# Kernel optimization log

Hardware: AMD Instinct MI355X
Metric: run time of the kernel (lower is better)

The kernel has to match this reference:

```python
import jax, jax.numpy as jnp
import numpy as np

N_NODES = 50000
N_EDGES = 800000
D = 128
E_DIM = 32
N_LAYERS = 4
BN_EPS = 1e-5


def setup_inputs() -> dict:
    key = jax.random.key(0)
    ks = jax.random.split(key, 9)
    return {
        "x": jax.random.normal(ks[0], (N_NODES, D), dtype=jnp.float32),
        "edge_attr": jax.random.normal(ks[1], (N_EDGES, E_DIM), dtype=jnp.float32),
        "edge_index": jax.random.randint(ks[2], (2, N_EDGES), 0, N_NODES, dtype=jnp.int64),
        "W_edge": jax.random.normal(ks[3], (N_LAYERS, E_DIM, D), dtype=jnp.float32) * 0.1,
        "b_edge": jnp.zeros((N_LAYERS, D), dtype=jnp.float32),
        "W1": jax.random.normal(ks[4], (N_LAYERS, D, D), dtype=jnp.float32) * 0.1,
        "b1": jnp.zeros((N_LAYERS, D), dtype=jnp.float32),
        "W2": jax.random.normal(ks[5], (N_LAYERS, D, D), dtype=jnp.float32) * 0.1,
        "b2": jnp.zeros((N_LAYERS, D), dtype=jnp.float32),
        "gamma": jnp.ones((N_LAYERS, D), dtype=jnp.float32),
        "beta": jnp.zeros((N_LAYERS, D), dtype=jnp.float32),
    }


def reference(x, edge_attr, edge_index, W_edge, b_edge, W1, b1, W2, b2, gamma, beta):
    src, dst = edge_index[0], edge_index[1]
    n = x.shape[0]
    for i in range(N_LAYERS):
        # GINEConv: message = ReLU(x_src + Lin(edge_attr)); scatter-add to dst
        e = edge_attr @ W_edge[i] + b_edge[i]            # [E, D]
        m = jax.nn.relu(x[src] + e)                      # [E, D]
        agg = jax.ops.segment_sum(m, dst, num_segments=n)  # [N, D]
        h = x + agg                                      # (1+eps)*x, eps=0
        # 2-layer MLP
        h = jax.nn.relu(h @ W1[i] + b1[i]) @ W2[i] + b2[i]
        # BatchNorm (training-mode batch stats, biased var) + ReLU; dropout off
        mean = h.mean(axis=0)
        var = h.var(axis=0)
        h = (h - mean) * jax.lax.rsqrt(var + BN_EPS) * gamma[i] + beta[i]
        x = jax.nn.relu(h)
    return x
```

## Files before the change

### kernel.cpp

```cpp
#include <hip/hip_runtime.h>

#define NN 50000
#define NE 800000
#define DD 128
#define ED 32
#define NL 4
#define BN_EPS 1e-5f
#define SCAN_B 1024
#define NB ((NN + SCAN_B - 1) / SCAN_B)
#define EB 128
#define MR 32

typedef __attribute__((ext_vector_type(8))) short bf16x8;
typedef __attribute__((ext_vector_type(4))) float f32x4;

__device__ __forceinline__ unsigned short f2bf(float f) {
    unsigned u = __float_as_uint(f);
    u += 0x7fffu + ((u >> 16) & 1u);
    return (unsigned short)(u >> 16);
}
__device__ __forceinline__ float bf2f(unsigned short h) {
    return __uint_as_float((unsigned)h << 16);
}

__global__ __launch_bounds__(256) void hist_kernel(
    const int* __restrict__ edst, int* __restrict__ deg)
{
    const int e = blockIdx.x * 256 + threadIdx.x;
    if (e < NE) atomicAdd(&deg[edst[e]], 1);
}

__global__ __launch_bounds__(256) void scan1_kernel(
    const int* __restrict__ deg, int* __restrict__ rowptr, int* __restrict__ bsum)
{
    __shared__ int sh[256];
    const int t = threadIdx.x, b = blockIdx.x;
    const int base = b * SCAN_B + t * 4;
    int v[4];
#pragma unroll
    for (int j = 0; j < 4; ++j) {
        const int idx = base + j;
        v[j] = (idx < NN) ? deg[idx] : 0;
    }
    sh[t] = v[0] + v[1] + v[2] + v[3];
    __syncthreads();
    for (int off = 1; off < 256; off <<= 1) {
        const int val = (t >= off) ? sh[t - off] : 0;
        __syncthreads();
        sh[t] += val;
        __syncthreads();
    }
    int p = (t == 0) ? 0 : sh[t - 1];
#pragma unroll
    for (int j = 0; j < 4; ++j) {
        const int idx = base + j;
        if (idx < NN) rowptr[idx] = p;
        p += v[j];
    }
    if (t == 255) bsum[b] = sh[255];
}

__global__ void scan2_kernel(int* __restrict__ bsum)
{
    if (threadIdx.x == 0) {
        int acc = 0;
        for (int i = 0; i < NB; ++i) { const int v = bsum[i]; bsum[i] = acc; acc += v; }
    }
}

__global__ __launch_bounds__(256) void scan3_kernel(
    int* __restrict__ rowptr, int* __restrict__ cursor, const int* __restrict__ bsum)
{
    const int idx = blockIdx.x * 256 + threadIdx.x;
    if (idx < NN) {
        const int v = rowptr[idx] + bsum[idx / SCAN_B];
        rowptr[idx] = v;
        cursor[idx] = v;
    }
    if (idx == 0) rowptr[NN] = NE;
}

__global__ __launch_bounds__(256) void scatter_kernel(
    const int* __restrict__ esrc, const int* __restrict__ edst,
    const float* __restrict__ ea, int* __restrict__ cursor,
    int2* __restrict__ sd_perm, unsigned short* __restrict__ ea_bf)
{
    const int e = blockIdx.x * 256 + threadIdx.x;
    if (e < NE) {
        const int d = edst[e];
        const int pos = atomicAdd(&cursor[d], 1);
        sd_perm[pos] = make_int2(esrc[e], d);
        const float* er = &ea[(size_t)e * ED];
        unsigned short* ob = &ea_bf[(size_t)pos * ED];
#pragma unroll
        for (int g = 0; g < 8; ++g) {
            const float4 v = *(const float4*)&er[g * 4];
            uint2 p;
            p.x = (unsigned)f2bf(v.x) | ((unsigned)f2bf(v.y) << 16);
            p.y = (unsigned)f2bf(v.z) | ((unsigned)f2bf(v.w) << 16);
            *(uint2*)&ob[g * 4] = p;
        }
    }
}

__global__ __launch_bounds__(256) void wconv_kernel(
    const float* __restrict__ We, unsigned short* __restrict__ wtb)
{
    const int tid = blockIdx.x * 256 + threadIdx.x;
    if (tid < NL * DD * ED) {
        const int l = tid / (DD * ED);
        const int r = tid % (DD * ED);
        const int c = r / ED, k = r % ED;
        wtb[tid] = f2bf(We[(size_t)l * ED * DD + k * DD + c]);
    }
}

__global__ __launch_bounds__(256) void w12conv_kernel(
    const float* __restrict__ W1, const float* __restrict__ W2,
    unsigned short* __restrict__ w1t, unsigned short* __restrict__ w2t)
{
    const int tid = blockIdx.x * 256 + threadIdx.x;
    if (tid < NL * DD * DD) {
        const int l = tid / (DD * DD);
        const int r = tid % (DD * DD);
        const int n = r / DD, k = r % DD;
        const size_t s = (size_t)l * DD * DD + k * DD + n;
        w1t[tid] = f2bf(W1[s]);
        w2t[tid] = f2bf(W2[s]);
    }
}

__global__ __launch_bounds__(256, 5) void edge_mfma_kernel(
    const float* __restrict__ x,
    const unsigned short* __restrict__ eab,
    const int2* __restrict__ sd_perm,
    const unsigned short* __restrict__ wtb,
    const float* __restrict__ be,
    float* __restrict__ agg)
{
    __shared__ unsigned short msgl[EB * 128];
    const int t = threadIdx.x;
    const int wv = t >> 6, ln = t & 63;
    const int l15 = ln & 15, kb = ln >> 4;
    const int e0 = blockIdx.x * EB;

    const int c0 = (2 * wv + 0) * 16 + l15;
    const int c1 = (2 * wv + 1) * 16 + l15;
    const bf16x8 bfr0 = *(const bf16x8*)&wtb[c0 * ED + kb * 8];
    const bf16x8 bfr1 = *(const bf16x8*)&wtb[c1 * ED + kb * 8];

#pragma unroll
    for (int eg = 0; eg < EB / 16; ++eg) {
        const int edge = eg * 16 + l15;
        const bf16x8 afr = *(const bf16x8*)&eab[(size_t)(e0 + edge) * ED + kb * 8];
        f32x4 z = {0.f, 0.f, 0.f, 0.f};
        const f32x4 d0 = __builtin_amdgcn_mfma_f32_16x16x32_bf16(afr, bfr0, z, 0, 0, 0);
        const f32x4 d1 = __builtin_amdgcn_mfma_f32_16x16x32_bf16(afr, bfr1, z, 0, 0, 0);
#pragma unroll
        for (int j = 0; j < 4; ++j) {
            const int mrow = eg * 16 + kb * 4 + j;
            const int sw = ((mrow >> 2) & 3) << 3;
            const int i0 = (((c0 >> 1) ^ sw) << 1) | (c0 & 1);
            const int i1 = (((c1 >> 1) ^ sw) << 1) | (c1 & 1);
            msgl[mrow * 128 + i0] = f2bf(d0[j]);
            msgl[mrow * 128 + i1] = f2bf(d1[j]);
        }
    }
    __syncthreads();

    const int lbase = wv * 32;
    const int2* sdp = &sd_perm[e0 + lbase];
    const int c2 = ln * 2;
    const float2 bv = *(const float2*)&be[c2];
    float2 acc = {0.f, 0.f};
    int seg_start = 0;
#pragma unroll 1
    for (int g = 0; g < 4; ++g) {
        const int gb = g * 8;
        int4 pr[4];
#pragma unroll
        for (int q = 0; q < 4; ++q)
            pr[q] = *(const int4*)&sdp[gb + 2 * q];
        const int srcs[8] = {pr[0].x, pr[0].z, pr[1].x, pr[1].z,
                             pr[2].x, pr[2].z, pr[3].x, pr[3].z};
        int dsts[9];
        dsts[0] = pr[0].y; dsts[1] = pr[0].w; dsts[2] = pr[1].y; dsts[3] = pr[1].w;
        dsts[4] = pr[2].y; dsts[5] = pr[2].w; dsts[6] = pr[3].y; dsts[7] = pr[3].w;
        dsts[8] = (gb + 8 < 32) ? sdp[gb + 8].y : -1;
        float2 xv[8];
#pragma unroll
        for (int q = 0; q < 8; ++q)
            xv[q] = *(const float2*)&x[(size_t)srcs[q] * DD + c2];
#pragma unroll
        for (int q = 0; q < 8; ++q) {
            const int i = gb + q;
            const int dw = ln ^ (((i >> 2) & 3) << 3);
            const unsigned mm = *(const unsigned*)&msgl[(lbase + i) * 128 + dw * 2];
            const float mlo = __uint_as_float(mm << 16);
            const float mhi = __uint_as_float(mm & 0xffff0000u);
            acc.x += fmaxf(xv[q].x + mlo + bv.x, 0.f);
            acc.y += fmaxf(xv[q].y + mhi + bv.y, 0.f);
            if (i == 31 || dsts[q + 1] != dsts[q]) {
                float* ap = &agg[(size_t)dsts[q] * DD + c2];
                if (seg_start > 0 && i < 31) {
                    *(float2*)ap = acc;
                } else {
                    unsafeAtomicAdd(ap + 0, acc.x);
                    unsafeAtomicAdd(ap + 1, acc.y);
                }
                acc.x = 0.f; acc.y = 0.f;
                seg_start = i + 1;
            }
        }
    }
}

__global__ __launch_bounds__(256, 5) void mlp_mfma_kernel(
    const float* __restrict__ x, const float* __restrict__ agg,
    float* __restrict__ h2out,
    const unsigned short* __restrict__ w1t,
    const unsigned short* __restrict__ w2t,
    const float* __restrict__ b1, const float* __restrict__ b2,
    float* __restrict__ bns)
{
    __shared__ unsigned short ah[MR * 128];
    __shared__ unsigned short al[MR * 128];
    __shared__ unsigned short bh[MR * 128];
    __shared__ unsigned short bl[MR * 128];
    const int t = threadIdx.x;
    const int wv = t >> 6, ln = t & 63, l15 = ln & 15, kb = ln >> 4;
    const int r0 = blockIdx.x * MR;

#pragma unroll
    for (int p = 0; p < 2; ++p) {
        const int row = p * 16 + (t >> 4);
        const int gc = t & 15;
        const int grow = r0 + row;
        float v[8] = {0.f, 0.f, 0.f, 0.f, 0.f, 0.f, 0.f, 0.f};
        if (grow < NN) {
            const size_t g = (size_t)grow * DD + gc * 8;
            const float4 xa = *(const float4*)&x[g];
            const float4 xc = *(const float4*)&x[g + 4];
            const float4 ga = *(const float4*)&agg[g];
            const float4 gc4 = *(const float4*)&agg[g + 4];
            v[0] = xa.x + ga.x; v[1] = xa.y + ga.y; v[2] = xa.z + ga.z; v[3] = xa.w + ga.w;
            v[4] = xc.x + gc4.x; v[5] = xc.y + gc4.y; v[6] = xc.z + gc4.z; v[7] = xc.w + gc4.w;
        }
        unsigned hiw[4], low[4];
#pragma unroll
        for (int j = 0; j < 4; ++j) {
            const unsigned short h0 = f2bf(v[2 * j]);
            const unsigned short h1 = f2bf(v[2 * j + 1]);
            const unsigned short q0 = f2bf(v[2 * j] - bf2f(h0));
            const unsigned short q1 = f2bf(v[2 * j + 1] - bf2f(h1));
            hiw[j] = (unsigned)h0 | ((unsigned)h1 << 16);
            low[j] = (unsigned)q0 | ((unsigned)q1 << 16);
        }
        const int off = row * 128 + (gc ^ (row & 7)) * 8;
        *(uint4*)&ah[off] = *(uint4*)hiw;
        *(uint4*)&al[off] = *(uint4*)low;
    }

    bf16x8 w1f[2][4];
#pragma unroll
    for (int nt = 0; nt < 2; ++nt) {
        const int n = wv * 32 + nt * 16 + l15;
#pragma unroll
        for (int ks = 0; ks < 4; ++ks)
            w1f[nt][ks] = *(const bf16x8*)&w1t[n * DD + ks * 32 + kb * 8];
    }
    const int cA = wv * 32 + l15, cB = wv * 32 + 16 + l15;
    const float b1v[2] = {b1[cA], b1[cB]};
    const float b2v[2] = {b2[cA], b2[cB]};
    __syncthreads();

    f32x4 acc[2][2];
#pragma unroll
    for (int mt = 0; mt < 2; ++mt)
#pragma unroll
        for (int nt = 0; nt < 2; ++nt)
            acc[mt][nt] = (f32x4){0.f, 0.f, 0.f, 0.f};
#pragma unroll
    for (int ks = 0; ks < 4; ++ks) {
#pragma unroll
        for (int mt = 0; mt < 2; ++mt) {
            const int row = mt * 16 + l15;
            const int off = row * 128 + ((ks * 4 + kb) ^ (row & 7)) * 8;
            const bf16x8 afh = *(const bf16x8*)&ah[off];
            const bf16x8 afl = *(const bf16x8*)&al[off];
#pragma unroll
            for (int nt = 0; nt < 2; ++nt) {
                acc[mt][nt] = __builtin_amdgcn_mfma_f32_16x16x32_bf16(afh, w1f[nt][ks], acc[mt][nt], 0, 0, 0);
                acc[mt][nt] = __builtin_amdgcn_mfma_f32_16x16x32_bf16(afl, w1f[nt][ks], acc[mt][nt], 0, 0, 0);
            }
        }
    }

#pragma unroll
    for (int mt = 0; mt < 2; ++mt) {
#pragma unroll
        for (int nt = 0; nt < 2; ++nt) {
            const int col = wv * 32 + nt * 16 + l15;
#pragma unroll
            for (int j = 0; j < 4; ++j) {
                const int row = mt * 16 + kb * 4 + j;
                const float v = fmaxf(acc[mt][nt][j] + b1v[nt], 0.f);
                const unsigned short hi = f2bf(v);
                const int off = row * 128 + ((col >> 3) ^ (row & 7)) * 8 + (col & 7);
                bh[off] = hi;
                bl[off] = f2bf(v - bf2f(hi));
            }
        }
    }

    bf16x8 w2f[2][4];
#pragma unroll
    for (int nt = 0; nt < 2; ++nt) {
        const int n = wv * 32 + nt * 16 + l15;
#pragma unroll
        for (int ks = 0; ks < 4; ++ks)
            w2f[nt][ks] = *(const bf16x8*)&w2t[n * DD + ks * 32 + kb * 8];
    }
    __syncthreads();

#pragma unroll
    for (int mt = 0; mt < 2; ++mt)
#pragma unroll
        for (int nt = 0; nt < 2; ++nt)
            acc[mt][nt] = (f32x4){0.f, 0.f, 0.f, 0.f};
#pragma unroll
    for (int ks = 0; ks < 4; ++ks) {
#pragma unroll
        for (int mt = 0; mt < 2; ++mt) {
            const int row = mt * 16 + l15;
            const int off = row * 128 + ((ks * 4 + kb) ^ (row & 7)) * 8;
            const bf16x8 afh = *(const bf16x8*)&bh[off];
            const bf16x8 afl = *(const bf16x8*)&bl[off];
#pragma unroll
            for (int nt = 0; nt < 2; ++nt) {
                acc[mt][nt] = __builtin_amdgcn_mfma_f32_16x16x32_bf16(afh, w2f[nt][ks], acc[mt][nt], 0, 0, 0);
                acc[mt][nt] = __builtin_amdgcn_mfma_f32_16x16x32_bf16(afl, w2f[nt][ks], acc[mt][nt], 0, 0, 0);
            }
        }
    }

    float ps[2] = {0.f, 0.f}, pq[2] = {0.f, 0.f};
#pragma unroll
    for (int mt = 0; mt < 2; ++mt) {
#pragma unroll
        for (int nt = 0; nt < 2; ++nt) {
            const int col = wv * 32 + nt * 16 + l15;
#pragma unroll
            for (int j = 0; j < 4; ++j) {
                const int row = r0 + mt * 16 + kb * 4 + j;
                const float v = acc[mt][nt][j] + b2v[nt];
                if (row < NN) {
                    h2out[(size_t)row * DD + col] = v;
                    ps[nt] += v;
                    pq[nt] += v * v;
                }
            }
        }
    }
#pragma unroll
    for (int nt = 0; nt < 2; ++nt) {
        ps[nt] += __shfl_xor(ps[nt], 16);
        ps[nt] += __shfl_xor(ps[nt], 32);
        pq[nt] += __shfl_xor(pq[nt], 16);
        pq[nt] += __shfl_xor(pq[nt], 32);
    }
    if (kb == 0) {
#pragma unroll
        for (int nt = 0; nt < 2; ++nt) {
            const int col = wv * 32 + nt * 16 + l15;
            unsafeAtomicAdd(&bns[col], ps[nt]);
            unsafeAtomicAdd(&bns[DD + col], pq[nt]);
        }
    }
}

__global__ __launch_bounds__(256) void bn_apply(
    const float* __restrict__ h2, const float* __restrict__ bns,
    const float* __restrict__ gamma, const float* __restrict__ beta,
    float* __restrict__ xout)
{
    const size_t i = ((size_t)blockIdx.x * 256 + threadIdx.x) * 4;
    if (i >= (size_t)NN * DD) return;
    const int c4 = (int)(i & 127);
    const float4 hv = *(const float4*)&h2[i];
    const float4 sv = *(const float4*)&bns[c4];
    const float4 qv = *(const float4*)&bns[DD + c4];
    const float4 gv = *(const float4*)&gamma[c4];
    const float4 bv = *(const float4*)&beta[c4];
    const float inv_n = 1.f / (float)NN;
    float4 ov;
    {
        const float m = sv.x * inv_n;
        const float var = qv.x * inv_n - m * m;
        ov.x = fmaxf((hv.x - m) * __frsqrt_rn(var + BN_EPS) * gv.x + bv.x, 0.f);
    }
    {
        const float m = sv.y * inv_n;
        const float var = qv.y * inv_n - m * m;
        ov.y = fmaxf((hv.y - m) * __frsqrt_rn(var + BN_EPS) * gv.y + bv.y, 0.f);
    }
    {
        const float m = sv.z * inv_n;
        const float var = qv.z * inv_n - m * m;
        ov.z = fmaxf((hv.z - m) * __frsqrt_rn(var + BN_EPS) * gv.z + bv.z, 0.f);
    }
    {
        const float m = sv.w * inv_n;
        const float var = qv.w * inv_n - m * m;
        ov.w = fmaxf((hv.w - m) * __frsqrt_rn(var + BN_EPS) * gv.w + bv.w, 0.f);
    }
    *(float4*)&xout[i] = ov;
}

extern "C" void kernel_launch(void* const* d_in, const int* in_sizes, int n_in,
                              void* d_out, int out_size, void* d_ws, size_t ws_size,
                              hipStream_t stream) {
    const float* x0    = (const float*)d_in[0];
    const float* ea    = (const float*)d_in[1];
    const int*   eidx  = (const int*)d_in[2];
    const float* We    = (const float*)d_in[3];
    const float* be    = (const float*)d_in[4];
    const float* W1    = (const float*)d_in[5];
    const float* b1    = (const float*)d_in[6];
    const float* W2    = (const float*)d_in[7];
    const float* b2    = (const float*)d_in[8];
    const float* gamma = (const float*)d_in[9];
    const float* beta  = (const float*)d_in[10];
    float* out = (float*)d_out;
    float* ws  = (float*)d_ws;

    float* agg = ws;
    float* xb  = agg + (size_t)NN * DD;
    float* bns = xb + (size_t)NN * DD;
    int* deg      = (int*)(bns + 256);
    int* rowptr   = deg + 50000;
    int* cursor   = rowptr + 50004;
    int* bsum     = cursor + 50000;
    int2* sd_perm = (int2*)(bsum + 64);
    unsigned short* ea_bf = (unsigned short*)(sd_perm + NE);
    unsigned short* wt_bf = ea_bf + (size_t)NE * ED;
    unsigned short* w1t   = wt_bf + (size_t)NL * DD * ED;
    unsigned short* w2t   = w1t + (size_t)NL * DD * DD;

    const int* esrc = eidx;
    const int* edst = eidx + NE;

    hipMemsetAsync(deg, 0, NN * sizeof(int), stream);
    hist_kernel<<<(NE + 255) / 256, 256, 0, stream>>>(edst, deg);
    scan1_kernel<<<NB, 256, 0, stream>>>(deg, rowptr, bsum);
    scan2_kernel<<<1, 64, 0, stream>>>(bsum);
    scan3_kernel<<<(NN + 255) / 256, 256, 0, stream>>>(rowptr, cursor, bsum);
    scatter_kernel<<<(NE + 255) / 256, 256, 0, stream>>>(
        esrc, edst, ea, cursor, sd_perm, ea_bf);
    wconv_kernel<<<(NL * DD * ED + 255) / 256, 256, 0, stream>>>(We, wt_bf);
    w12conv_kernel<<<(NL * DD * DD + 255) / 256, 256, 0, stream>>>(W1, W2, w1t, w2t);

    const float* xcur = x0;
    for (int l = 0; l < NL; ++l) {
        hipMemsetAsync(agg, 0, (size_t)NN * DD * sizeof(float), stream);
        hipMemsetAsync(bns, 0, 2 * DD * sizeof(float), stream);
        edge_mfma_kernel<<<NE / EB, 256, 0, stream>>>(
            xcur, ea_bf, sd_perm,
            wt_bf + (size_t)l * DD * ED, be + (size_t)l * DD, agg);
        mlp_mfma_kernel<<<(NN + MR - 1) / MR, 256, 0, stream>>>(
            xcur, agg, agg,
            w1t + (size_t)l * DD * DD, w2t + (size_t)l * DD * DD,
            b1 + (size_t)l * DD, b2 + (size_t)l * DD, bns);
        float* xn = (l == NL - 1) ? out : xb;
        bn_apply<<<(NN * DD / 4 + 255) / 256, 256, 0, stream>>>(
            agg, bns, gamma + (size_t)l * DD, beta + (size_t)l * DD, xn);
        xcur = xn;
    }
}
```

Baseline: 714.3 us.

## Store node features in bf16 and split edge-attr permutation into gather pass

Node features between layers are now stored as bf16, so the random per-edge source gathers in the edge kernel and the row reads in the MLP kernel move half the bytes. The final layer still writes fp32 output. The edge-attribute permutation is split into an index scatter plus a separate coalesced gather kernel that uses eight threads per edge. This adds two extra kernels and lowers the precision of inputs to each layer, which risks accuracy drift across four layers.

```diff
diff --git a/kernel.cpp b/kernel.cpp
--- a/kernel.cpp
+++ b/kernel.cpp
@@ -80,27 +80,48 @@
     if (idx == 0) rowptr[NN] = NE;
 }
 
-__global__ __launch_bounds__(256) void scatter_kernel(
+__global__ __launch_bounds__(256) void scatter_idx_kernel(
     const int* __restrict__ esrc, const int* __restrict__ edst,
-    const float* __restrict__ ea, int* __restrict__ cursor,
-    int2* __restrict__ sd_perm, unsigned short* __restrict__ ea_bf)
+    int* __restrict__ cursor, int2* __restrict__ sd_perm, int* __restrict__ eid_perm)
 {
     const int e = blockIdx.x * 256 + threadIdx.x;
     if (e < NE) {
         const int d = edst[e];
         const int pos = atomicAdd(&cursor[d], 1);
         sd_perm[pos] = make_int2(esrc[e], d);
-        const float* er = &ea[(size_t)e * ED];
-        unsigned short* ob = &ea_bf[(size_t)pos * ED];
-#pragma unroll
-        for (int g = 0; g < 8; ++g) {
-            const float4 v = *(const float4*)&er[g * 4];
-            uint2 p;
-            p.x = (unsigned)f2bf(v.x) | ((unsigned)f2bf(v.y) << 16);
-            p.y = (unsigned)f2bf(v.z) | ((unsigned)f2bf(v.w) << 16);
-            *(uint2*)&ob[g * 4] = p;
-        }
-    }
+        eid_perm[pos] = e;
+    }
+}
+
+__global__ __launch_bounds__(256) void ea_gather_kernel(
+    const float* __restrict__ ea, const int* __restrict__ eid_perm,
+    unsigned short* __restrict__ ea_bf)
+{
+    const int tid = blockIdx.x * 256 + threadIdx.x;
+    const int pos = tid >> 3, j = tid & 7;
+    if (pos < NE) {
+        const int e = eid_perm[pos];
+        const float4 v = *(const float4*)&ea[(size_t)e * ED + j * 4];
+        uint2 p;
+        p.x = (unsigned)f2bf(v.x) | ((unsigned)f2bf(v.y) << 16);
+        p.y = (unsigned)f2bf(v.z) | ((unsigned)f2bf(v.w) << 16);
+        *(uint2*)&ea_bf[(size_t)pos * ED + j * 4] = p;
+    }
+}
+
+__global__ __launch_bounds__(256) void x0conv_kernel(
+    const float* __restrict__ x0, unsigned short* __restrict__ xbf)
+{
+    const size_t i = ((size_t)blockIdx.x * 256 + threadIdx.x) * 8;
+    if (i >= (size_t)NN * DD) return;
+    const float4 a = *(const float4*)&x0[i];
+    const float4 b = *(const float4*)&x0[i + 4];
+    uint4 o;
+    o.x = (unsigned)f2bf(a.x) | ((unsigned)f2bf(a.y) << 16);
+    o.y = (unsigned)f2bf(a.z) | ((unsigned)f2bf(a.w) << 16);
+    o.z = (unsigned)f2bf(b.x) | ((unsigned)f2bf(b.y) << 16);
+    o.w = (unsigned)f2bf(b.z) | ((unsigned)f2bf(b.w) << 16);
+    *(uint4*)&xbf[i] = o;
 }
 
 __global__ __launch_bounds__(256) void wconv_kernel(
@@ -131,7 +152,7 @@
 }
 
 __global__ __launch_bounds__(256, 5) void edge_mfma_kernel(
-    const float* __restrict__ x,
+    const unsigned short* __restrict__ xbf,
     const unsigned short* __restrict__ eab,
     const int2* __restrict__ sd_perm,
     const unsigned short* __restrict__ wtb,
@@ -189,8 +210,11 @@
         dsts[8] = (gb + 8 < 32) ? sdp[gb + 8].y : -1;
         float2 xv[8];
 #pragma unroll
-        for (int q = 0; q < 8; ++q)
-            xv[q] = *(const float2*)&x[(size_t)srcs[q] * DD + c2];
+        for (int q = 0; q < 8; ++q) {
+            const unsigned xu = *(const unsigned*)&xbf[(size_t)srcs[q] * DD + c2];
+            xv[q].x = __uint_as_float(xu << 16);
+            xv[q].y = __uint_as_float(xu & 0xffff0000u);
+        }
 #pragma unroll
         for (int q = 0; q < 8; ++q) {
             const int i = gb + q;
@@ -216,7 +240,7 @@
 }
 
 __global__ __launch_bounds__(256, 5) void mlp_mfma_kernel(
-    const float* __restrict__ x, const float* __restrict__ agg,
+    const unsigned short* __restrict__ xbf, const float* __restrict__ agg,
     float* __restrict__ h2out,
     const unsigned short* __restrict__ w1t,
     const unsigned short* __restrict__ w2t,
@@ -239,12 +263,17 @@
         float v[8] = {0.f, 0.f, 0.f, 0.f, 0.f, 0.f, 0.f, 0.f};
         if (grow < NN) {
             const size_t g = (size_t)grow * DD + gc * 8;
-            const float4 xa = *(const float4*)&x[g];
-            const float4 xc = *(const float4*)&x[g + 4];
+            const uint4 xu = *(const uint4*)&xbf[g];
             const float4 ga = *(const float4*)&agg[g];
-            const float4 gc4 = *(const float4*)&agg[g + 4];
-            v[0] = xa.x + ga.x; v[1] = xa.y + ga.y; v[2] = xa.z + ga.z; v[3] = xa.w + ga.w;
-            v[4] = xc.x + gc4.x; v[5] = xc.y + gc4.y; v[6] = xc.z + gc4.z; v[7] = xc.w + gc4.w;
+            const float4 gb4 = *(const float4*)&agg[g + 4];
+            v[0] = __uint_as_float(xu.x << 16)          + ga.x;
+            v[1] = __uint_as_float(xu.x & 0xffff0000u)  + ga.y;
+            v[2] = __uint_as_float(xu.y << 16)          + ga.z;
+            v[3] = __uint_as_float(xu.y & 0xffff0000u)  + ga.w;
+            v[4] = __uint_as_float(xu.z << 16)          + gb4.x;
+            v[5] = __uint_as_float(xu.z & 0xffff0000u)  + gb4.y;
+            v[6] = __uint_as_float(xu.w << 16)          + gb4.z;
+            v[7] = __uint_as_float(xu.w & 0xffff0000u)  + gb4.w;
         }
         unsigned hiw[4], low[4];
 #pragma unroll
@@ -379,7 +408,36 @@
     }
 }
 
-__global__ __launch_bounds__(256) void bn_apply(
+__global__ __launch_bounds__(256) void bn_apply_bf16(
+    const float* __restrict__ h2, const float* __restrict__ bns,
+    const float* __restrict__ gamma, const float* __restrict__ beta,
+    unsigned short* __restrict__ xout)
+{
+    const size_t i = ((size_t)blockIdx.x * 256 + threadIdx.x) * 4;
+    if (i >= (size_t)NN * DD) return;
+    const int c4 = (int)(i & 127);
+    const float4 hv = *(const float4*)&h2[i];
+    const float4 sv = *(const float4*)&bns[c4];
+    const float4 qv = *(const float4*)&bns[DD + c4];
+    const float4 gv = *(const float4*)&gamma[c4];
+    const float4 bv = *(const float4*)&beta[c4];
+    const float inv_n = 1.f / (float)NN;
+    float o0, o1, o2, o3;
+    { const float m = sv.x * inv_n; const float var = qv.x * inv_n - m * m;
+      o0 = fmaxf((hv.x - m) * __frsqrt_rn(var + BN_EPS) * gv.x + bv.x, 0.f); }
+    { const float m = sv.y * inv_n; const float var = qv.y * inv_n - m * m;
+      o1 = fmaxf((hv.y - m) * __frsqrt_rn(var + BN_EPS) * gv.y + bv.y, 0.f); }
+    { const float m = sv.z * inv_n; const float var = qv.z * inv_n - m * m;
+      o2 = fmaxf((hv.z - m) * __frsqrt_rn(var + BN_EPS) * gv.z + bv.z, 0.f); }
+    { const float m = sv.w * inv_n; const float var = qv.w * inv_n - m * m;
+      o3 = fmaxf((hv.w - m) * __frsqrt_rn(var + BN_EPS) * gv.w + bv.w, 0.f); }
+    uint2 o;
+    o.x = (unsigned)f2bf(o0) | ((unsigned)f2bf(o1) << 16);
+    o.y = (unsigned)f2bf(o2) | ((unsigned)f2bf(o3) << 16);
+    *(uint2*)&xout[i] = o;
+}
+
+__global__ __launch_bounds__(256) void bn_apply_f32(
     const float* __restrict__ h2, const float* __restrict__ bns,
     const float* __restrict__ gamma, const float* __restrict__ beta,
     float* __restrict__ xout)
@@ -394,26 +452,14 @@
     const float4 bv = *(const float4*)&beta[c4];
     const float inv_n = 1.f / (float)NN;
     float4 ov;
-    {
-        const float m = sv.x * inv_n;
-        const float var = qv.x * inv_n - m * m;
-        ov.x = fmaxf((hv.x - m) * __frsqrt_rn(var + BN_EPS) * gv.x + bv.x, 0.f);
-    }
-    {
-        const float m = sv.y * inv_n;
-        const float var = qv.y * inv_n - m * m;
-        ov.y = fmaxf((hv.y - m) * __frsqrt_rn(var + BN_EPS) * gv.y + bv.y, 0.f);
-    }
-    {
-        const float m = sv.z * inv_n;
-        const float var = qv.z * inv_n - m * m;
-        ov.z = fmaxf((hv.z - m) * __frsqrt_rn(var + BN_EPS) * gv.z + bv.z, 0.f);
-    }
-    {
-        const float m = sv.w * inv_n;
-        const float var = qv.w * inv_n - m * m;
-        ov.w = fmaxf((hv.w - m) * __frsqrt_rn(var + BN_EPS) * gv.w + bv.w, 0.f);
-    }
+    { const float m = sv.x * inv_n; const float var = qv.x * inv_n - m * m;
+      ov.x = fmaxf((hv.x - m) * __frsqrt_rn(var + BN_EPS) * gv.x + bv.x, 0.f); }
+    { const float m = sv.y * inv_n; const float var = qv.y * inv_n - m * m;
+      ov.y = fmaxf((hv.y - m) * __frsqrt_rn(var + BN_EPS) * gv.y + bv.y, 0.f); }
+    { const float m = sv.z * inv_n; const float var = qv.z * inv_n - m * m;
+      ov.z = fmaxf((hv.z - m) * __frsqrt_rn(var + BN_EPS) * gv.z + bv.z, 0.f); }
+    { const float m = sv.w * inv_n; const float var = qv.w * inv_n - m * m;
+      ov.w = fmaxf((hv.w - m) * __frsqrt_rn(var + BN_EPS) * gv.w + bv.w, 0.f); }
     *(float4*)&xout[i] = ov;
 }
 
@@ -435,17 +481,18 @@
     float* ws  = (float*)d_ws;
 
     float* agg = ws;
-    float* xb  = agg + (size_t)NN * DD;
-    float* bns = xb + (size_t)NN * DD;
+    float* bns = agg + (size_t)NN * DD;
     int* deg      = (int*)(bns + 256);
     int* rowptr   = deg + 50000;
     int* cursor   = rowptr + 50004;
     int* bsum     = cursor + 50000;
     int2* sd_perm = (int2*)(bsum + 64);
-    unsigned short* ea_bf = (unsigned short*)(sd_perm + NE);
+    int* eid_perm = (int*)(sd_perm + NE);
+    unsigned short* ea_bf = (unsigned short*)(eid_perm + NE);
     unsigned short* wt_bf = ea_bf + (size_t)NE * ED;
     unsigned short* w1t   = wt_bf + (size_t)NL * DD * ED;
     unsigned short* w2t   = w1t + (size_t)NL * DD * DD;
+    unsigned short* xbf   = w2t + (size_t)NL * DD * DD;
 
     const int* esrc = eidx;
     const int* edst = eidx + NE;
@@ -455,25 +502,29 @@
     scan1_kernel<<<NB, 256, 0, stream>>>(deg, rowptr, bsum);
     scan2_kernel<<<1, 64, 0, stream>>>(bsum);
     scan3_kernel<<<(NN + 255) / 256, 256, 0, stream>>>(rowptr, cursor, bsum);
-    scatter_kernel<<<(NE + 255) / 256, 256, 0, stream>>>(
-        esrc, edst, ea, cursor, sd_perm, ea_bf);
+    scatter_idx_kernel<<<(NE + 255) / 256, 256, 0, stream>>>(
+        esrc, edst, cursor, sd_perm, eid_perm);
+    ea_gather_kernel<<<(NE * 8 + 255) / 256, 256, 0, stream>>>(ea, eid_perm, ea_bf);
+    x0conv_kernel<<<((NN * DD / 8) + 255) / 256, 256, 0, stream>>>(x0, xbf);
     wconv_kernel<<<(NL * DD * ED + 255) / 256, 256, 0, stream>>>(We, wt_bf);
     w12conv_kernel<<<(NL * DD * DD + 255) / 256, 256, 0, stream>>>(W1, W2, w1t, w2t);
 
-    const float* xcur = x0;
     for (int l = 0; l < NL; ++l) {
         hipMemsetAsync(agg, 0, (size_t)NN * DD * sizeof(float), stream);
         hipMemsetAsync(bns, 0, 2 * DD * sizeof(float), stream);
         edge_mfma_kernel<<<NE / EB, 256, 0, stream>>>(
-            xcur, ea_bf, sd_perm,
+            xbf, ea_bf, sd_perm,
             wt_bf + (size_t)l * DD * ED, be + (size_t)l * DD, agg);
         mlp_mfma_kernel<<<(NN + MR - 1) / MR, 256, 0, stream>>>(
-            xcur, agg, agg,
+            xbf, agg, agg,
             w1t + (size_t)l * DD * DD, w2t + (size_t)l * DD * DD,
             b1 + (size_t)l * DD, b2 + (size_t)l * DD, bns);
-        float* xn = (l == NL - 1) ? out : xb;
-        bn_apply<<<(NN * DD / 4 + 255) / 256, 256, 0, stream>>>(
-            agg, bns, gamma + (size_t)l * DD, beta + (size_t)l * DD, xn);
-        xcur = xn;
-    }
-}
+        if (l < NL - 1) {
+            bn_apply_bf16<<<(NN * DD / 4 + 255) / 256, 256, 0, stream>>>(
+                agg, bns, gamma + (size_t)l * DD, beta + (size_t)l * DD, xbf);
+        } else {
+            bn_apply_f32<<<(NN * DD / 4 + 255) / 256, 256, 0, stream>>>(
+                agg, bns, gamma + (size_t)l * DD, beta + (size_t)l * DD, out);
+        }
+    }
+}
```

New measurement: 669.7 us. -6.2%, faster.
